# Optimization experiments

Hardware: AMD Instinct MI355X
Metric: run time of the kernel (lower is better)

Reference implementation:

```python
import jax, jax.numpy as jnp
import numpy as np

H = 64; DS = 32; DT = 24; ED = 16; OUT = 2
N = 10000       # nodes per type
E = 40000       # edges per edge type (before self loops)
MAX_DEG = 12    # static padded neighbor-sequence length (PyG to_dense_batch max); excess dropped


def setup_inputs() -> dict:
    key = jax.random.key(0)
    k = iter(jax.random.split(key, 40))
    def lin(o, i):
        s = 1.0 / np.sqrt(i)
        return jax.random.uniform(next(k), (o, i), jnp.float32, -s, s)
    inp = {}
    inp["x_source"] = jax.random.normal(next(k), (N, DS), jnp.float32)
    inp["x_target"] = jax.random.normal(next(k), (N, DT), jnp.float32)
    # 4 edge types in order [src->src, tgt->tgt, src->tgt, tgt->src], each [2, E]
    inp["edges"] = jax.random.randint(next(k), (4, 2, E), 0, N, dtype=jnp.int32)
    inp["edge_attr_st"] = jax.random.normal(next(k), (E, ED), jnp.float32)
    # node encoders (Linear-ReLU-Dropout(eval)-Linear)
    inp["We_s1"] = lin(H, DS); inp["be_s1"] = jnp.zeros((H,), jnp.float32)
    inp["We_s2"] = lin(H, H);  inp["be_s2"] = jnp.zeros((H,), jnp.float32)
    inp["We_t1"] = lin(H, DT); inp["be_t1"] = jnp.zeros((H,), jnp.float32)
    inp["We_t2"] = lin(H, H);  inp["be_t2"] = jnp.zeros((H,), jnp.float32)
    # 12 SAGEConv(aggr='lstm') blocks: 3 layers x 4 edge types, stacked on dim 0
    s = 1.0 / np.sqrt(H)
    inp["Wih"] = jax.random.uniform(next(k), (12, 4 * H, H), jnp.float32, -s, s)
    inp["Whh"] = jax.random.uniform(next(k), (12, 4 * H, H), jnp.float32, -s, s)
    inp["bih"] = jax.random.uniform(next(k), (12, 4 * H), jnp.float32, -s, s)
    inp["bhh"] = jax.random.uniform(next(k), (12, 4 * H), jnp.float32, -s, s)
    inp["Wl"]  = jax.random.uniform(next(k), (12, H, H), jnp.float32, -s, s)
    inp["bl"]  = jnp.zeros((12, H), jnp.float32)
    inp["Wr"]  = jax.random.uniform(next(k), (12, H, H), jnp.float32, -s, s)
    # edge gate + edge MLP head
    inp["Wg1"] = lin(H, 2 * H);   inp["bg1"] = jnp.zeros((H,), jnp.float32)
    inp["Wg2"] = lin(1, H);       inp["bg2"] = jnp.zeros((1,), jnp.float32)
    inp["Wm1"] = lin(H, H + ED);  inp["bm1"] = jnp.zeros((H,), jnp.float32)
    inp["Wm2"] = lin(H // 2, H);  inp["bm2"] = jnp.zeros((H // 2,), jnp.float32)
    inp["Wm3"] = lin(OUT, H // 2); inp["bm3"] = jnp.zeros((OUT,), jnp.float32)
    return inp


def _lstm_last(dense, Wih, Whh, bih, bhh):
    # dense: [n, T, H] padded neighbor sequences; PyG LSTMAggregation returns lstm(x)[0][:, -1]
    n = dense.shape[0]
    h0 = jnp.zeros((n, H), dense.dtype)
    def step(carry, x_t):
        h, c = carry
        g = x_t @ Wih.T + bih + h @ Whh.T + bhh  # torch gate order: i, f, g, o
        i, f, gg, o = jnp.split(g, 4, axis=-1)
        c = jax.nn.sigmoid(f) * c + jax.nn.sigmoid(i) * jnp.tanh(gg)
        h = jax.nn.sigmoid(o) * jnp.tanh(c)
        return (h, c), None
    (h, _), _ = jax.lax.scan(step, (h0, h0), jnp.swapaxes(dense, 0, 1))
    return h


def _sage_lstm(x_src, x_dst, src, dst, Wih, Whh, bih, bhh, Wl, bl, Wr):
    n_src, n_dst = x_src.shape[0], x_dst.shape[0]
    # add_self_loops(num_nodes=n_dst): appends (i, i) for every destination node, zero edge_attr
    loop = jnp.arange(n_dst, dtype=src.dtype)
    src = jnp.concatenate([src, loop]); dst = jnp.concatenate([dst, loop])
    # sort_edge_index(sort_by_row=False): stable lexicographic (dst, src) order
    order = jnp.argsort(dst.astype(jnp.int64) * n_src + src.astype(jnp.int64))
    src_s, dst_s = src[order], dst[order]
    xj = x_src[src_s]                                   # gather neighbor feats [E', H]
    deg = jnp.zeros((n_dst,), jnp.int32).at[dst_s].add(1)
    start = jnp.cumsum(deg) - deg                       # CSR row starts
    pos = jnp.arange(dst_s.shape[0], dtype=jnp.int32) - start[dst_s]
    dense = jnp.zeros((n_dst, MAX_DEG, x_src.shape[1]), x_src.dtype)
    dense = dense.at[dst_s, pos].set(xj, mode="drop")   # pad-to-dense, drop beyond MAX_DEG
    agg = _lstm_last(dense, Wih, Whh, bih, bhh)
    # SAGEConv: lin_l(aggr) + lin_r(x_root); lin_r has no bias
    return agg @ Wl.T + bl + x_dst @ Wr.T


def reference(x_source, x_target, edges, edge_attr_st,
              We_s1, be_s1, We_s2, be_s2, We_t1, be_t1, We_t2, be_t2,
              Wih, Whh, bih, bhh, Wl, bl, Wr,
              Wg1, bg1, Wg2, bg2, Wm1, bm1, Wm2, bm2, Wm3, bm3):
    relu = jax.nn.relu
    xs = relu(x_source @ We_s1.T + be_s1) @ We_s2.T + be_s2
    xt = relu(x_target @ We_t1.T + be_t1) @ We_t2.T + be_t2

    def layer(xs, xt, L):
        specs = [(xs, xs, 0), (xt, xt, 1), (xs, xt, 2), (xt, xs, 3)]
        outs = []
        for x_src, x_dst, et in specs:
            i = L * 4 + et
            outs.append(_sage_lstm(x_src, x_dst, edges[et, 0], edges[et, 1],
                                   Wih[i], Whh[i], bih[i], bhh[i], Wl[i], bl[i], Wr[i]))
        # HeteroConv(aggr='mean'): each node type receives from exactly 2 edge types
        return 0.5 * (outs[0] + outs[3]), 0.5 * (outs[1] + outs[2])

    s1, t1 = layer(xs, xt, 0); s1, t1 = relu(s1), relu(t1)
    s2, t2 = layer(s1, t1, 1); s2, t2 = relu(s2 + s1), relu(t2 + t1)
    s3, t3 = layer(s2, t2, 2); s3, t3 = relu(s3 + s2), relu(t3 + t2)

    # edge head on the main ('source','to','target') edges (original edges, no self loops)
    se, te = s3[edges[2, 0]], t3[edges[2, 1]]
    g = jax.nn.sigmoid(relu(jnp.concatenate([se, te], -1) @ Wg1.T + bg1) @ Wg2.T + bg2)
    er = g * se + (1.0 - g) * te
    h = relu(jnp.concatenate([er, edge_attr_st], -1) @ Wm1.T + bm1)
    h = relu(h @ Wm2.T + bm2)
    return h @ Wm3.T + bm3  # [E, OUT] edge logits
```

## Files before the change

### kernel.cpp

```cpp
#include <hip/hip_runtime.h>

#define N_NODES 10000
#define N_EDGES 40000
#define HD 64
#define MAXD 12
#define CAP 32
#define Y2ROW ((size_t)(N_NODES + 1) * 128)
#define LOG2E 1.44269504f
#define XST 148

typedef __attribute__((ext_vector_type(8))) short short8;
typedef __attribute__((ext_vector_type(4))) float floatx4;

#define MFMA16(A, B, C) __builtin_amdgcn_mfma_f32_16x16x32_bf16(A, B, C, 0, 0, 0)

#if __has_builtin(__builtin_amdgcn_exp2f)
#define EXP2(x) __builtin_amdgcn_exp2f(x)
#else
#define EXP2(x) __expf((x) * 0.6931471806f)
#endif

__device__ __forceinline__ float sigmoidf_(float x) {
  return 1.0f / (1.0f + __expf(-x));
}
__device__ __forceinline__ float fma4(float4 w, float4 x, float a) {
  a = fmaf(w.x, x.x, a);
  a = fmaf(w.y, x.y, a);
  a = fmaf(w.z, x.z, a);
  return fmaf(w.w, x.w, a);
}

__device__ __forceinline__ void split_frag(float4 a, float4 b, short8& hi, short8& lo) {
  float f[8] = {a.x, a.y, a.z, a.w, b.x, b.y, b.z, b.w};
  union { short8 v; unsigned d[4]; } H, L;
#pragma unroll
  for (int p = 0; p < 4; ++p) {
    unsigned u0 = __float_as_uint(f[2 * p]);
    unsigned u1 = __float_as_uint(f[2 * p + 1]);
    H.d[p] = (u0 >> 16) | (u1 & 0xFFFF0000u);
    float l0 = f[2 * p] - __uint_as_float(u0 & 0xFFFF0000u);
    float l1 = f[2 * p + 1] - __uint_as_float(u1 & 0xFFFF0000u);
    L.d[p] = (__float_as_uint(l0) >> 16) | (__float_as_uint(l1) & 0xFFFF0000u);
  }
  hi = H.v;
  lo = L.v;
}


__global__ void scatter_kernel(const int* __restrict__ edges, int* __restrict__ cnt,
                               int* __restrict__ pool) {
  int idx = blockIdx.x * 256 + threadIdx.x;
  if (idx >= 4 * N_EDGES) return;
  int et = idx / N_EDGES, e = idx - et * N_EDGES;
  int src = edges[(et * 2) * N_EDGES + e];
  int dst = edges[(et * 2 + 1) * N_EDGES + e];
  int slot = atomicAdd(&cnt[et * N_NODES + dst], 1);
  if (slot < CAP) pool[(et * N_NODES + dst) * CAP + slot] = src;
}

__global__ void sortrows_kernel(const int* __restrict__ cnt, const int* __restrict__ pool,
                                int* __restrict__ nbr) {
  __shared__ int buf[64][CAP + 1];
  int idx = blockIdx.x * 64 + threadIdx.x;
  if (idx >= 4 * N_NODES) return;
  int n = idx % N_NODES;
  int c = cnt[idx];
  if (c > CAP) c = CAP;
  int* a = buf[threadIdx.x];
  const int* row = pool + idx * CAP;
  for (int j = 0; j < c; ++j) a[j] = row[j] * 2;
  a[c] = n * 2 + 1;
  ++c;
  for (int i2 = 1; i2 < c; ++i2) {
    int key = a[i2];
    int b = i2 - 1;
    while (b >= 0 && a[b] > key) { a[b + 1] = a[b]; --b; }
    a[b + 1] = key;
  }
  int* onbr = nbr + idx * MAXD;
  for (int t = 0; t < MAXD; ++t) onbr[t] = (t < c) ? (a[t] >> 1) : N_NODES;
}


__device__ __forceinline__ void wfrag_body(const float* __restrict__ W,
                                           short* __restrict__ w16, int gid) {
  int lane = gid & 63;
  int combo = gid >> 6;
  int kc = combo & 1;
  int g = (combo >> 1) & 3;
  int w = (combo >> 3) & 3;
  int i = combo >> 5;
  float sc = (g == 2) ? (2.0f * LOG2E) : LOG2E;
  int gate = g * 64 + w * 16 + (lane & 15);
  int k0 = kc * 32 + (lane >> 4) * 8;
  const float* src = W + ((size_t)i * 256 + gate) * 64 + k0;
  float4 a = ((const float4*)src)[0];
  float4 b = ((const float4*)src)[1];
  a.x *= sc; a.y *= sc; a.z *= sc; a.w *= sc;
  b.x *= sc; b.y *= sc; b.z *= sc; b.w *= sc;
  short8 hi, lo;
  split_frag(a, b, hi, lo);
  short8* dst = (short8*)w16;
  dst[(combo * 2 + 0) * 64 + lane] = hi;
  dst[(combo * 2 + 1) * 64 + lane] = lo;
}

__device__ __forceinline__ void wfrag_body_noscale(const float* __restrict__ W,
                                                   short* __restrict__ w16, int gid) {
  int lane = gid & 63;
  int combo = gid >> 6;
  int kc = combo & 1;
  int g = (combo >> 1) & 3;
  int w = (combo >> 3) & 3;
  int i = combo >> 5;
  int gate = g * 64 + w * 16 + (lane & 15);
  int k0 = kc * 32 + (lane >> 4) * 8;
  const float* src = W + ((size_t)i * 256 + gate) * 64 + k0;
  float4 a = ((const float4*)src)[0];
  float4 b = ((const float4*)src)[1];
  short8 hi, lo;
  split_frag(a, b, hi, lo);
  short8* dst = (short8*)w16;
  dst[(combo * 2 + 0) * 64 + lane] = hi;
  dst[(combo * 2 + 1) * 64 + lane] = lo;
}

__device__ __forceinline__ void cw_body(const float* __restrict__ Wl,
    const float* __restrict__ Wr, short* __restrict__ cw, int gid) {
  int lane = gid & 63;
  int rest = gid >> 6;
  int combo = rest & 7;
  int mat = (rest >> 3) % 3;
  int pair = rest / 24;
  int L = pair >> 1, side = pair & 1;
  int iA = L * 4 + (side ? 1 : 0);
  int iB = L * 4 + (side ? 2 : 3);
  int wp = combo >> 1, kc = combo & 1;
  int row = wp * 16 + (lane & 15);
  int k0 = kc * 32 + (lane >> 4) * 8;
  float4 a, b;
  if (mat == 0) {
    const float* s = Wl + ((size_t)iA * 64 + row) * 64 + k0;
    a = ((const float4*)s)[0]; b = ((const float4*)s)[1];
  } else if (mat == 1) {
    const float* s = Wl + ((size_t)iB * 64 + row) * 64 + k0;
    a = ((const float4*)s)[0]; b = ((const float4*)s)[1];
  } else {
    const float* sA = Wr + ((size_t)iA * 64 + row) * 64 + k0;
    const float* sB = Wr + ((size_t)iB * 64 + row) * 64 + k0;
    float4 a1 = ((const float4*)sA)[0], b1 = ((const float4*)sA)[1];
    float4 a2 = ((const float4*)sB)[0], b2 = ((const float4*)sB)[1];
    a.x = a1.x + a2.x; a.y = a1.y + a2.y; a.z = a1.z + a2.z; a.w = a1.w + a2.w;
    b.x = b1.x + b2.x; b.y = b1.y + b2.y; b.z = b1.z + b2.z; b.w = b1.w + b2.w;
  }
  short8 hi, lo;
  split_frag(a, b, hi, lo);
  short8* dst = (short8*)cw;
  int base = ((pair * 3 + mat) * 8 + combo) * 2;
  dst[(base + 0) * 64 + lane] = hi;
  dst[(base + 1) * 64 + lane] = lo;
}

__device__ __forceinline__ void eh_body(const float* __restrict__ Wg1,
    const float* __restrict__ Wm1, const float* __restrict__ Wm2,
    short* __restrict__ ehw16, int gid) {
  int lane = gid & 63;
  int combo = gid >> 6;
  int n = lane & 15, quad = lane >> 4;
  int mat, wp, kc;
  if (combo < 16) { mat = 0; wp = combo >> 2; kc = combo & 3; }
  else if (combo < 28) { int c2 = combo - 16; mat = 1; wp = c2 / 3; kc = c2 % 3; }
  else { int c2 = combo - 28; mat = 2; wp = c2 >> 1; kc = c2 & 1; }
  int row = wp * 16 + n;
  int k0 = kc * 32 + quad * 8;
  float4 a = {0.f, 0.f, 0.f, 0.f}, b = {0.f, 0.f, 0.f, 0.f};
  if (mat == 0) {
    const float* s = Wg1 + (size_t)row * 128 + k0;
    a = ((const float4*)s)[0]; b = ((const float4*)s)[1];
  } else if (mat == 1) {
    if (k0 + 8 <= 80) {
      const float* s = Wm1 + (size_t)row * 80 + k0;
      a = ((const float4*)s)[0]; b = ((const float4*)s)[1];
    }
  } else {
    const float* s = Wm2 + (size_t)row * 64 + k0;
    a = ((const float4*)s)[0]; b = ((const float4*)s)[1];
  }
  short8 hi, lo;
  split_frag(a, b, hi, lo);
  short8* dst = (short8*)ehw16;
  dst[(combo * 2 + 0) * 64 + lane] = hi;
  dst[(combo * 2 + 1) * 64 + lane] = lo;
}

__global__ __launch_bounds__(256) void prep_all_kernel(
    const float* __restrict__ Whh, const float* __restrict__ Wih,
    const float* __restrict__ Wl, const float* __restrict__ Wr,
    const float* __restrict__ Wg1, const float* __restrict__ Wm1,
    const float* __restrict__ Wm2,
    short* __restrict__ whh16, short* __restrict__ wih16, short* __restrict__ cw16,
    short* __restrict__ ehw16, unsigned* __restrict__ ybase) {
  int gid = blockIdx.x * 256 + threadIdx.x;
  if (gid < 24576) {
    wfrag_body(Whh, whh16, gid);
  } else if (gid < 49152) {
    wfrag_body_noscale(Wih, wih16, gid - 24576);
  } else if (gid < 58368) {
    cw_body(Wl, Wr, cw16, gid - 49152);
  } else if (gid < 60416) {
    eh_body(Wg1, Wm1, Wm2, ehw16, gid - 58368);
  } else if (gid < 60928) {
    int t = gid - 60416;
    int et = t >> 7, col = t & 127;
    ybase[(size_t)et * Y2ROW + (size_t)N_NODES * 128 + col] = 0u;
  }
}


template <int IN>
__device__ __forceinline__ void encode_body(const float* __restrict__ x,
    const float* __restrict__ W1, const float* __restrict__ b1,
    const float* __restrict__ W2, const float* __restrict__ b2, float* __restrict__ out) {
  __shared__ float xs[4][IN];
  __shared__ float h1[4][HD];
  int w = threadIdx.x >> 6, l = threadIdx.x & 63;
  int n = blockIdx.x * 4 + w;
  if (l < IN) xs[w][l] = x[n * IN + l];
  __syncthreads();
  float acc = b1[l];
#pragma unroll
  for (int k = 0; k < IN; ++k) acc = fmaf(xs[w][k], W1[l * IN + k], acc);
  h1[w][l] = fmaxf(acc, 0.0f);
  __syncthreads();
  float acc2 = b2[l];
#pragma unroll
  for (int k = 0; k < HD; ++k) acc2 = fmaf(h1[w][k], W2[l * HD + k], acc2);
  out[n * HD + l] = acc2;
}

__global__ __launch_bounds__(256) void encode_both_kernel(
    const float* __restrict__ xs0, const float* __restrict__ xt0,
    const float* __restrict__ Ws1, const float* __restrict__ bs1,
    const float* __restrict__ Ws2, const float* __restrict__ bs2,
    const float* __restrict__ Wt1, const float* __restrict__ bt1,
    const float* __restrict__ Wt2, const float* __restrict__ bt2,
    float* __restrict__ outS, float* __restrict__ outT) {
  if (blockIdx.y == 0) encode_body<32>(xs0, Ws1, bs1, Ws2, bs2, outS);
  else encode_body<24>(xt0, Wt1, bt1, Wt2, bt2, outT);
}


__global__ __launch_bounds__(256) void ygemm_mfma_kernel(const float* __restrict__ xs0,
    const float* __restrict__ xt0, const short* __restrict__ wih16L, unsigned* __restrict__ ybase) {
  __shared__ __align__(16) float xS[16][68];
  __shared__ __align__(16) float pS[16][260];
  int et = blockIdx.y;
  const float* x = (et == 0 || et == 2) ? xs0 : xt0;
  const short8* wf = (const short8*)(wih16L + (size_t)et * 32768);
  unsigned* y = ybase + (size_t)et * Y2ROW;
  int tid = threadIdx.x, w = tid >> 6, l = tid & 63;
  int quad = l >> 4, n = l & 15;
  int n0 = blockIdx.x * 16;
  {
    int node = tid >> 4, f4 = tid & 15;
    float4 v = *(const float4*)(x + (size_t)(n0 + node) * 64 + f4 * 4);
    *(float4*)&xS[node][f4 * 4] = v;
  }
  short8 Bh[4][2], Bl[4][2];
#pragma unroll
  for (int wp = 0; wp < 4; ++wp)
#pragma unroll
    for (int kc = 0; kc < 2; ++kc) {
      int combo = (wp * 4 + w) * 2 + kc;
      Bh[wp][kc] = wf[(combo * 2 + 0) * 64 + l];
      Bl[wp][kc] = wf[(combo * 2 + 1) * 64 + l];
    }
  __syncthreads();
  short8 Ah[2], Al[2];
  {
    const float* hp = &xS[n][quad * 8];
    float4 q0 = *(const float4*)hp, q1 = *(const float4*)(hp + 4);
    float4 q2 = *(const float4*)(hp + 32), q3 = *(const float4*)(hp + 36);
    split_frag(q0, q1, Ah[0], Al[0]);
    split_frag(q2, q3, Ah[1], Al[1]);
  }
  floatx4 acc[4];
#pragma unroll
  for (int wp = 0; wp < 4; ++wp) {
    floatx4 a = {0.f, 0.f, 0.f, 0.f};
    a = MFMA16(Ah[0], Bh[wp][0], a);
    a = MFMA16(Ah[1], Bh[wp][1], a);
    a = MFMA16(Al[0], Bh[wp][0], a);
    a = MFMA16(Al[1], Bh[wp][1], a);
    a = MFMA16(Ah[0], Bl[wp][0], a);
    a = MFMA16(Ah[1], Bl[wp][1], a);
    acc[wp] = a;
  }
#pragma unroll
  for (int wp = 0; wp < 4; ++wp)
#pragma unroll
    for (int r = 0; r < 4; ++r)
      pS[quad * 4 + r][(wp * 16 + n) * 4 + w] = acc[wp][r];
  __syncthreads();
#pragma unroll
  for (int cc = 0; cc < 4; ++cc) {
    int g4 = cc * 256 + tid;
    int node = g4 >> 6, u = g4 & 63;
    const float* p = &pS[node][u * 4];
    unsigned r0 = __float_as_uint(p[0]) + 0x8000u;
    unsigned r1 = __float_as_uint(p[1]) + 0x8000u;
    unsigned r2 = __float_as_uint(p[2]) + 0x8000u;
    unsigned r3 = __float_as_uint(p[3]) + 0x8000u;
    uint2 v;
    v.x = __builtin_amdgcn_perm(r1, r0, 0x07060302u);
    v.y = __builtin_amdgcn_perm(r3, r2, 0x07060302u);
    ((uint2*)(y + (size_t)(n0 + node) * 128))[u] = v;
  }
}


__global__ __launch_bounds__(256) void lstm_mfma_kernel(const int* __restrict__ nbrAll,
    const unsigned* __restrict__ ybase, const short* __restrict__ whh16L,
    const float* __restrict__ bihL, const float* __restrict__ bhhL, float* __restrict__ aggBase) {
  __shared__ __align__(16) unsigned pkS[2][16 * 68];
  __shared__ int nbS[16][MAXD];
  int et = blockIdx.y;
  const int* nbr = nbrAll + (size_t)et * N_NODES * MAXD;
  const uint2* y2 = (const uint2*)(ybase + (size_t)et * Y2ROW);
  const short* whh16 = whh16L + (size_t)et * 32768;
  const float* bih = bihL + et * 256;
  const float* bhh = bhhL + et * 256;
  float* agg = aggBase + (size_t)et * N_NODES * HD;
  int tid = threadIdx.x, w = tid >> 6, l = tid & 63;
  int quad = l >> 4, n = l & 15, u = w * 16 + n;
  int n0 = blockIdx.x * 16;
  if (tid < 16 * MAXD) ((int*)nbS)[tid] = nbr[n0 * MAXD + tid];
  short8 Bh[4][2], Bl[4][2];
  {
    const short8* wf = (const short8*)whh16;
#pragma unroll
    for (int g = 0; g < 4; ++g)
#pragma unroll
      for (int kc = 0; kc < 2; ++kc) {
        int combo = (w * 4 + g) * 2 + kc;
        Bh[g][kc] = wf[(combo * 2 + 0) * 64 + l];
        Bl[g][kc] = wf[(combo * 2 + 1) * 64 + l];
      }
  }
  float bs[4];
#pragma unroll
  for (int g = 0; g < 4; ++g)
    bs[g] = (bih[g * 64 + u] + bhh[g * 64 + u]) * ((g == 2) ? (2.0f * LOG2E) : LOG2E);
  float c[4] = {0.f, 0.f, 0.f, 0.f}, h[4];
  short8 Ah[2], Al[2];
#pragma unroll
  for (int kc = 0; kc < 2; ++kc) { Ah[kc] = (short8)0; Al[kc] = (short8)0; }
  __syncthreads();
  uint2 Y[4];
#pragma unroll
  for (int r = 0; r < 4; ++r) Y[r] = y2[(size_t)nbS[quad * 4 + r][0] * 64 + u];
  for (int t = 0; t < MAXD; ++t) {
    float yg[4][4];
#pragma unroll
    for (int r = 0; r < 4; ++r) {
      yg[0][r] = __uint_as_float(Y[r].x << 16);
      yg[1][r] = __uint_as_float(Y[r].x & 0xFFFF0000u);
      yg[2][r] = __uint_as_float(Y[r].y << 16);
      yg[3][r] = __uint_as_float(Y[r].y & 0xFFFF0000u);
    }
    floatx4 acc[4];
#pragma unroll
    for (int g = 0; g < 4; ++g) {
      floatx4 a = {yg[g][0], yg[g][1], yg[g][2], yg[g][3]};
      a = MFMA16(Ah[0], Bh[g][0], a);
      a = MFMA16(Ah[1], Bh[g][1], a);
      a = MFMA16(Al[0], Bh[g][0], a);
      a = MFMA16(Al[1], Bh[g][1], a);
      a = MFMA16(Ah[0], Bl[g][0], a);
      a = MFMA16(Ah[1], Bl[g][1], a);
      acc[g] = a;
    }
    if (t + 1 < MAXD) {
#pragma unroll
      for (int r = 0; r < 4; ++r) Y[r] = y2[(size_t)nbS[quad * 4 + r][t + 1] * 64 + u];
    }
    int buf = (t + 1) & 1;
#pragma unroll
    for (int r = 0; r < 4; ++r) {
      float gi = acc[0][r] + bs[0];
      float gf = acc[1][r] + bs[1];
      float gg = acc[2][r] + bs[2];
      float go = acc[3][r] + bs[3];
      float a_ = EXP2(-gi);
      float b_ = EXP2(fminf(-gg, 60.f));
      float f_ = EXP2(-gf);
      float o_ = EXP2(-go);
      float p1 = 1.f + a_, p2 = 1.f + b_, p3 = 1.f + f_;
      float d1 = p1 * p2;
      float num = fmaf(c[r], d1, (1.f - b_) * p3);
      c[r] = num * __builtin_amdgcn_rcpf(p3 * d1);
      float e_ = EXP2(c[r] * (-2.0f * LOG2E));
      h[r] = (1.f - e_) * __builtin_amdgcn_rcpf((1.f + e_) * (1.f + o_));
      unsigned ub = __float_as_uint(h[r]);
      float lo = h[r] - __uint_as_float(ub & 0xFFFF0000u);
      pkS[buf][(quad * 4 + r) * 68 + u] =
          __builtin_amdgcn_perm(ub, __float_as_uint(lo), 0x07060302u);
    }
    __syncthreads();
    if (t + 1 < MAXD) {
#pragma unroll
      for (int kc = 0; kc < 2; ++kc) {
        const unsigned* pb = &pkS[buf][n * 68 + kc * 32 + quad * 8];
        uint4 qa = *(const uint4*)pb;
        uint4 qb = *(const uint4*)(pb + 4);
        union { short8 s; unsigned d[4]; } H, L;
        H.d[0] = __builtin_amdgcn_perm(qa.y, qa.x, 0x07060302u);
        H.d[1] = __builtin_amdgcn_perm(qa.w, qa.z, 0x07060302u);
        H.d[2] = __builtin_amdgcn_perm(qb.y, qb.x, 0x07060302u);
        H.d[3] = __builtin_amdgcn_perm(qb.w, qb.z, 0x07060302u);
        L.d[0] = __builtin_amdgcn_perm(qa.y, qa.x, 0x05040100u);
        L.d[1] = __builtin_amdgcn_perm(qa.w, qa.z, 0x05040100u);
        L.d[2] = __builtin_amdgcn_perm(qb.y, qb.x, 0x05040100u);
        L.d[3] = __builtin_amdgcn_perm(qb.w, qb.z, 0x05040100u);
        Ah[kc] = H.s;
        Al[kc] = L.s;
      }
    }
  }
#pragma unroll
  for (int r = 0; r < 4; ++r)
    agg[(size_t)(n0 + quad * 4 + r) * HD + u] = h[r];
}


__global__ __launch_bounds__(256) void combine_mfma_kernel(const float* __restrict__ aggBase,
    const short* __restrict__ cwL, const float* __restrict__ blL,
    const float* __restrict__ xS0, const float* __restrict__ xT0, int has_res,
    float* __restrict__ outS, float* __restrict__ outT) {
  __shared__ __align__(16) float tS[3][16][68];
  int side = blockIdx.y;
  int etA = side ? 1 : 0, etB = side ? 2 : 3;
  const float* srcs[3];
  srcs[0] = aggBase + (size_t)etA * N_NODES * HD;
  srcs[1] = aggBase + (size_t)etB * N_NODES * HD;
  srcs[2] = side ? xT0 : xS0;
  float* out = side ? outT : outS;
  const short8* wf = (const short8*)cwL + (size_t)side * 3072;
  const float* blA = blL + etA * 64;
  const float* blB = blL + etB * 64;
  int tid = threadIdx.x, w = tid >> 6, l = tid & 63;
  int quad = l >> 4, n = l & 15;
  int n0 = blockIdx.x * 16;
  {
    int node = tid >> 4, f4 = tid & 15;
#pragma unroll
    for (int m = 0; m < 3; ++m) {
      float4 v = *(const float4*)(srcs[m] + (size_t)(n0 + node) * 64 + f4 * 4);
      *(float4*)&tS[m][node][f4 * 4] = v;
    }
  }
  short8 Bh[3][2], Bl[3][2];
#pragma unroll
  for (int m = 0; m < 3; ++m)
#pragma unroll
    for (int kc = 0; kc < 2; ++kc) {
      int base = (m * 8 + w * 2 + kc) * 2;
      Bh[m][kc] = wf[(base + 0) * 64 + l];
      Bl[m][kc] = wf[(base + 1) * 64 + l];
    }
  float bsum = blA[w * 16 + n] + blB[w * 16 + n];
  __syncthreads();
  floatx4 a = {0.f, 0.f, 0.f, 0.f};
#pragma unroll
  for (int m = 0; m < 3; ++m) {
    short8 Ah[2], Al[2];
    const float* hp = &tS[m][n][quad * 8];
    float4 q0 = *(const float4*)hp, q1 = *(const float4*)(hp + 4);
    float4 q2 = *(const float4*)(hp + 32), q3 = *(const float4*)(hp + 36);
    split_frag(q0, q1, Ah[0], Al[0]);
    split_frag(q2, q3, Ah[1], Al[1]);
    a = MFMA16(Ah[0], Bh[m][0], a);
    a = MFMA16(Ah[1], Bh[m][1], a);
    a = MFMA16(Al[0], Bh[m][0], a);
    a = MFMA16(Al[1], Bh[m][1], a);
    a = MFMA16(Ah[0], Bl[m][0], a);
    a = MFMA16(Ah[1], Bl[m][1], a);
  }
#pragma unroll
  for (int r = 0; r < 4; ++r) {
    int node = quad * 4 + r;
    float v = 0.5f * (a[r] + bsum);
    if (has_res) v += tS[2][node][w * 16 + n];
    out[(size_t)(n0 + node) * 64 + w * 16 + n] = fmaxf(v, 0.f);
  }
}


__global__ __launch_bounds__(256) void edge_head_mfma_kernel(
    const int* __restrict__ esrc, const int* __restrict__ edst, const float* __restrict__ ea,
    const float* __restrict__ s3, const float* __restrict__ t3,
    const short* __restrict__ ehw16,
    const float* __restrict__ bg1, const float* __restrict__ Wg2,
    const float* __restrict__ bg2, const float* __restrict__ bm1,
    const float* __restrict__ bm2, const float* __restrict__ Wm3,
    const float* __restrict__ bm3, float* __restrict__ out) {
  __shared__ __align__(16) float xS[64][XST];
  __shared__ float gP[4][64];
  int tid = threadIdx.x, w = tid >> 6, l = tid & 63;
  int quad = l >> 4, n = l & 15;
  int e0 = blockIdx.x * 64;
  const short8* wf = (const short8*)ehw16;
  for (int idx = tid; idx < 2048; idx += 256) {
    int e = idx >> 5, kk = idx & 31;
    float4 v;
    if (kk < 16) v = ((const float4*)(s3 + (size_t)esrc[e0 + e] * 64))[kk];
    else         v = ((const float4*)(t3 + (size_t)edst[e0 + e] * 64))[kk - 16];
    *(float4*)&xS[e][kk * 4] = v;
  }
  {
    int e = tid >> 2, kk = tid & 3;
    *(float4*)&xS[e][128 + kk * 4] = ((const float4*)(ea + (size_t)(e0 + e) * 16))[kk];
  }
  __syncthreads();
  {
    short8 Bh[4], Bl[4];
#pragma unroll
    for (int kc = 0; kc < 4; ++kc) {
      int cb = w * 4 + kc;
      Bh[kc] = wf[(cb * 2 + 0) * 64 + l];
      Bl[kc] = wf[(cb * 2 + 1) * 64 + l];
    }
    float bg = bg1[w * 16 + n];
    float wg2l = Wg2[w * 16 + n];
    float red[4][4];
#pragma unroll
    for (int mt = 0; mt < 4; ++mt) {
      floatx4 a = {bg, bg, bg, bg};
#pragma unroll
      for (int kc = 0; kc < 4; ++kc) {
        const float* hp = &xS[mt * 16 + n][kc * 32 + quad * 8];
        float4 q0 = *(const float4*)hp, q1 = *(const float4*)(hp + 4);
        short8 Ah, Al;
        split_frag(q0, q1, Ah, Al);
        a = MFMA16(Ah, Bh[kc], a);
        a = MFMA16(Al, Bh[kc], a);
        a = MFMA16(Ah, Bl[kc], a);
      }
#pragma unroll
      for (int r = 0; r < 4; ++r) red[mt][r] = fmaxf(a[r], 0.f) * wg2l;
    }
#pragma unroll
    for (int mt = 0; mt < 4; ++mt)
#pragma unroll
      for (int r = 0; r < 4; ++r) {
#pragma unroll
        for (int off = 1; off < 16; off <<= 1)
          red[mt][r] += __shfl_xor(red[mt][r], off);
      }
#pragma unroll
    for (int mt = 0; mt < 4; ++mt)
#pragma unroll
      for (int r = 0; r < 4; ++r)
        if (n == mt * 4 + r) gP[w][mt * 16 + quad * 4 + r] = red[mt][r];
  }
  __syncthreads();
  float gv[4];
  {
    float b2 = bg2[0];
#pragma unroll
    for (int mt = 0; mt < 4; ++mt) {
      int e = mt * 16 + n;
      float p = gP[0][e] + gP[1][e] + gP[2][e] + gP[3][e] + b2;
      gv[mt] = sigmoidf_(p);
    }
  }
  floatx4 acc2[4];
  {
    short8 Bh[3], Bl[3];
#pragma unroll
    for (int kc = 0; kc < 3; ++kc) {
      int cb = 16 + w * 3 + kc;
      Bh[kc] = wf[(cb * 2 + 0) * 64 + l];
      Bl[kc] = wf[(cb * 2 + 1) * 64 + l];
    }
    float bm = bm1[w * 16 + n];
#pragma unroll
    for (int mt = 0; mt < 4; ++mt) {
      int e = mt * 16 + n;
      float g = gv[mt];
      floatx4 a = {bm, bm, bm, bm};
#pragma unroll
      for (int kc = 0; kc < 2; ++kc) {
        const float* sp = &xS[e][kc * 32 + quad * 8];
        float4 s0 = *(const float4*)sp, s1 = *(const float4*)(sp + 4);
        float4 t0 = *(const float4*)(sp + 64), t1 = *(const float4*)(sp + 68);
        float4 e0v, e1v;
        e0v.x = fmaf(g, s0.x - t0.x, t0.x); e0v.y = fmaf(g, s0.y - t0.y, t0.y);
        e0v.z = fmaf(g, s0.z - t0.z, t0.z); e0v.w = fmaf(g, s0.w - t0.w, t0.w);
        e1v.x = fmaf(g, s1.x - t1.x, t1.x); e1v.y = fmaf(g, s1.y - t1.y, t1.y);
        e1v.z = fmaf(g, s1.z - t1.z, t1.z); e1v.w = fmaf(g, s1.w - t1.w, t1.w);
        short8 Ah, Al;
        split_frag(e0v, e1v, Ah, Al);
        a = MFMA16(Ah, Bh[kc], a);
        a = MFMA16(Al, Bh[kc], a);
        a = MFMA16(Ah, Bl[kc], a);
      }
      {
        float4 z0 = {0.f, 0.f, 0.f, 0.f}, z1 = {0.f, 0.f, 0.f, 0.f};
        if (quad < 2) {
          const float* ap = &xS[e][128 + quad * 8];
          z0 = *(const float4*)ap;
          z1 = *(const float4*)(ap + 4);
        }
        short8 Ah, Al;
        split_frag(z0, z1, Ah, Al);
        a = MFMA16(Ah, Bh[2], a);
        a = MFMA16(Al, Bh[2], a);
        a = MFMA16(Ah, Bl[2], a);
      }
      acc2[mt] = a;
    }
  }
  __syncthreads();
#pragma unroll
  for (int mt = 0; mt < 4; ++mt)
#pragma unroll
    for (int r = 0; r < 4; ++r)
      xS[mt * 16 + quad * 4 + r][w * 16 + n] = fmaxf(acc2[mt][r], 0.f);
  __syncthreads();
  {
    int s = w & 1, mtb = (w >> 1) * 2;
    short8 Bh[2], Bl[2];
#pragma unroll
    for (int kc = 0; kc < 2; ++kc) {
      int cb = 28 + s * 2 + kc;
      Bh[kc] = wf[(cb * 2 + 0) * 64 + l];
      Bl[kc] = wf[(cb * 2 + 1) * 64 + l];
    }
    float bm = bm2[s * 16 + n];
#pragma unroll
    for (int mi = 0; mi < 2; ++mi) {
      int mt = mtb + mi;
      int e = mt * 16 + n;
      floatx4 a = {bm, bm, bm, bm};
#pragma unroll
      for (int kc = 0; kc < 2; ++kc) {
        const float* sp = &xS[e][kc * 32 + quad * 8];
        float4 q0 = *(const float4*)sp, q1 = *(const float4*)(sp + 4);
        short8 Ah, Al;
        split_frag(q0, q1, Ah, Al);
        a = MFMA16(Ah, Bh[kc], a);
        a = MFMA16(Al, Bh[kc], a);
        a = MFMA16(Ah, Bl[kc], a);
      }
#pragma unroll
      for (int r = 0; r < 4; ++r)
        xS[mt * 16 + quad * 4 + r][64 + s * 16 + n] = fmaxf(a[r], 0.f);
    }
  }
  __syncthreads();
  if (tid < 128) {
    int e = tid >> 1, j = tid & 1;
    const float4* hp = (const float4*)&xS[e][64];
    const float4* w3 = (const float4*)(Wm3 + j * 32);
    float a = bm3[j];
#pragma unroll
    for (int kk = 0; kk < 8; ++kk) a = fma4(w3[kk], hp[kk], a);
    out[(e0 + e) * 2 + j] = a;
  }
}


extern "C" void kernel_launch(void* const* d_in, const int* in_sizes, int n_in, void* d_out,
                              int out_size, void* d_ws, size_t ws_size, hipStream_t stream) {
  const float* x_source = (const float*)d_in[0];
  const float* x_target = (const float*)d_in[1];
  const int* edges = (const int*)d_in[2];
  const float* edge_attr = (const float*)d_in[3];
  const float* We_s1 = (const float*)d_in[4];
  const float* be_s1 = (const float*)d_in[5];
  const float* We_s2 = (const float*)d_in[6];
  const float* be_s2 = (const float*)d_in[7];
  const float* We_t1 = (const float*)d_in[8];
  const float* be_t1 = (const float*)d_in[9];
  const float* We_t2 = (const float*)d_in[10];
  const float* be_t2 = (const float*)d_in[11];
  const float* Wih = (const float*)d_in[12];
  const float* Whh = (const float*)d_in[13];
  const float* bih = (const float*)d_in[14];
  const float* bhh = (const float*)d_in[15];
  const float* Wl = (const float*)d_in[16];
  const float* bl = (const float*)d_in[17];
  const float* Wr = (const float*)d_in[18];
  const float* Wg1 = (const float*)d_in[19];
  const float* bg1 = (const float*)d_in[20];
  const float* Wg2 = (const float*)d_in[21];
  const float* bg2 = (const float*)d_in[22];
  const float* Wm1 = (const float*)d_in[23];
  const float* bm1 = (const float*)d_in[24];
  const float* Wm2 = (const float*)d_in[25];
  const float* bm2 = (const float*)d_in[26];
  const float* Wm3 = (const float*)d_in[27];
  const float* bm3 = (const float*)d_in[28];
  float* out = (float*)d_out;

  int* nbr = (int*)d_ws;
  int* cnt = nbr + 4 * N_NODES * MAXD;
  int* pool = cnt + 4 * N_NODES;
  float* fb = (float*)(pool + 4 * N_NODES * CAP);
  float* bufS[2] = {fb, fb + N_NODES * HD};
  float* bufT[2] = {fb + 2 * N_NODES * HD, fb + 3 * N_NODES * HD};
  float* aggBase = fb + (size_t)4 * N_NODES * HD;
  unsigned* y4 = (unsigned*)(fb + (size_t)8 * N_NODES * HD);
  short* whh16 = (short*)(y4 + 4 * Y2ROW);
  short* wih16 = whh16 + 12 * 32768;
  short* cw16 = wih16 + 12 * 32768;
  short* ehw16 = cw16 + 6 * 24576;

  hipMemsetAsync(cnt, 0, 4 * N_NODES * sizeof(int), stream);
  prep_all_kernel<<<240, 256, 0, stream>>>(Whh, Wih, Wl, Wr, Wg1, Wm1, Wm2,
      whh16, wih16, cw16, ehw16, y4);
  scatter_kernel<<<(4 * N_EDGES + 255) / 256, 256, 0, stream>>>(edges, cnt, pool);
  sortrows_kernel<<<(4 * N_NODES + 63) / 64, 64, 0, stream>>>(cnt, pool, nbr);
  encode_both_kernel<<<dim3(N_NODES / 4, 2), 256, 0, stream>>>(x_source, x_target,
      We_s1, be_s1, We_s2, be_s2, We_t1, be_t1, We_t2, be_t2, bufS[0], bufT[0]);

  int cur = 0;
  for (int L = 0; L < 3; ++L) {
    ygemm_mfma_kernel<<<dim3(N_NODES / 16, 4), 256, 0, stream>>>(bufS[cur], bufT[cur],
        wih16 + (size_t)L * 4 * 32768, y4);
    lstm_mfma_kernel<<<dim3(N_NODES / 16, 4), 256, 0, stream>>>(nbr, y4,
        whh16 + (size_t)L * 4 * 32768, bih + L * 1024, bhh + L * 1024, aggBase);
    combine_mfma_kernel<<<dim3(N_NODES / 16, 2), 256, 0, stream>>>(aggBase,
        cw16 + (size_t)L * 2 * 24576, bl + L * 256,
        bufS[cur], bufT[cur], L > 0 ? 1 : 0, bufS[1 - cur], bufT[1 - cur]);
    cur = 1 - cur;
  }

  edge_head_mfma_kernel<<<N_EDGES / 64, 256, 0, stream>>>(edges + 4 * N_EDGES,
      edges + 5 * N_EDGES, edge_attr, bufS[cur], bufT[cur], ehw16,
      bg1, Wg2, bg2, bm1, bm2, Wm3, bm3, out);
}
```

Before: 450.2 us.

## Split LSTM recurrent MFMA chain, defer neighbor load, fold memset into prep kernel

```diff
diff --git a/kernel.cpp b/kernel.cpp
--- a/kernel.cpp
+++ b/kernel.cpp
@@ -199,7 +199,7 @@
     const float* __restrict__ Wg1, const float* __restrict__ Wm1,
     const float* __restrict__ Wm2,
     short* __restrict__ whh16, short* __restrict__ wih16, short* __restrict__ cw16,
-    short* __restrict__ ehw16, unsigned* __restrict__ ybase) {
+    short* __restrict__ ehw16, unsigned* __restrict__ ybase, int* __restrict__ cnt) {
   int gid = blockIdx.x * 256 + threadIdx.x;
   if (gid < 24576) {
     wfrag_body(Whh, whh16, gid);
@@ -213,6 +213,8 @@
     int t = gid - 60416;
     int et = t >> 7, col = t & 127;
     ybase[(size_t)et * Y2ROW + (size_t)N_NODES * 128 + col] = 0u;
+  } else if (gid < 60928 + 4 * N_NODES) {
+    cnt[gid - 60928] = 0;
   }
 }
 
@@ -360,6 +362,19 @@
 #pragma unroll
   for (int r = 0; r < 4; ++r) Y[r] = y2[(size_t)nbS[quad * 4 + r][0] * 64 + u];
   for (int t = 0; t < MAXD; ++t) {
+    floatx4 acc[4];
+#pragma unroll
+    for (int g = 0; g < 4; ++g) {
+      floatx4 a1 = {0.f, 0.f, 0.f, 0.f};
+      floatx4 a2 = {0.f, 0.f, 0.f, 0.f};
+      a1 = MFMA16(Ah[0], Bh[g][0], a1);
+      a1 = MFMA16(Ah[1], Bh[g][1], a1);
+      a1 = MFMA16(Al[0], Bh[g][0], a1);
+      a2 = MFMA16(Al[1], Bh[g][1], a2);
+      a2 = MFMA16(Ah[0], Bl[g][0], a2);
+      a2 = MFMA16(Ah[1], Bl[g][1], a2);
+      acc[g] = a1 + a2;
+    }
     float yg[4][4];
 #pragma unroll
     for (int r = 0; r < 4; ++r) {
@@ -368,29 +383,13 @@
       yg[2][r] = __uint_as_float(Y[r].y << 16);
       yg[3][r] = __uint_as_float(Y[r].y & 0xFFFF0000u);
     }
-    floatx4 acc[4];
-#pragma unroll
-    for (int g = 0; g < 4; ++g) {
-      floatx4 a = {yg[g][0], yg[g][1], yg[g][2], yg[g][3]};
-      a = MFMA16(Ah[0], Bh[g][0], a);
-      a = MFMA16(Ah[1], Bh[g][1], a);
-      a = MFMA16(Al[0], Bh[g][0], a);
-      a = MFMA16(Al[1], Bh[g][1], a);
-      a = MFMA16(Ah[0], Bl[g][0], a);
-      a = MFMA16(Ah[1], Bl[g][1], a);
-      acc[g] = a;
-    }
-    if (t + 1 < MAXD) {
-#pragma unroll
-      for (int r = 0; r < 4; ++r) Y[r] = y2[(size_t)nbS[quad * 4 + r][t + 1] * 64 + u];
-    }
     int buf = (t + 1) & 1;
 #pragma unroll
     for (int r = 0; r < 4; ++r) {
-      float gi = acc[0][r] + bs[0];
-      float gf = acc[1][r] + bs[1];
-      float gg = acc[2][r] + bs[2];
-      float go = acc[3][r] + bs[3];
+      float gi = acc[0][r] + (yg[0][r] + bs[0]);
+      float gf = acc[1][r] + (yg[1][r] + bs[1]);
+      float gg = acc[2][r] + (yg[2][r] + bs[2]);
+      float go = acc[3][r] + (yg[3][r] + bs[3]);
       float a_ = EXP2(-gi);
       float b_ = EXP2(fminf(-gg, 60.f));
       float f_ = EXP2(-gf);
@@ -406,8 +405,10 @@
       pkS[buf][(quad * 4 + r) * 68 + u] =
           __builtin_amdgcn_perm(ub, __float_as_uint(lo), 0x07060302u);
     }
-    __syncthreads();
     if (t + 1 < MAXD) {
+      __syncthreads();
+#pragma unroll
+      for (int r = 0; r < 4; ++r) Y[r] = y2[(size_t)nbS[quad * 4 + r][t + 1] * 64 + u];
 #pragma unroll
       for (int kc = 0; kc < 2; ++kc) {
         const unsigned* pb = &pkS[buf][n * 68 + kc * 32 + quad * 8];
@@ -717,9 +718,8 @@
   short* cw16 = wih16 + 12 * 32768;
   short* ehw16 = cw16 + 6 * 24576;
 
-  hipMemsetAsync(cnt, 0, 4 * N_NODES * sizeof(int), stream);
-  prep_all_kernel<<<240, 256, 0, stream>>>(Whh, Wih, Wl, Wr, Wg1, Wm1, Wm2,
-      whh16, wih16, cw16, ehw16, y4);
+  prep_all_kernel<<<(60928 + 4 * N_NODES + 255) / 256, 256, 0, stream>>>(
+      Whh, Wih, Wl, Wr, Wg1, Wm1, Wm2, whh16, wih16, cw16, ehw16, y4, cnt);
   scatter_kernel<<<(4 * N_EDGES + 255) / 256, 256, 0, stream>>>(edges, cnt, pool);
   sortrows_kernel<<<(4 * N_NODES + 63) / 64, 64, 0, stream>>>(cnt, pool, nbr);
   encode_both_kernel<<<dim3(N_NODES / 4, 2), 256, 0, stream>>>(x_source, x_target,
```

Result: slower. 469.5 us (+4.3%).
